# Performance work log

Measured on AMD Instinct MI355X. Metric: run time of the kernel, lower is better.

The kernel has to match this reference:

```python
import jax, jax.numpy as jnp
import numpy as np

DIM = 1024
HEADS = 16
DIM_HEAD = 64
INNER = HEADS * DIM_HEAD
N = 60  # 7 region tokens + 53 channel tokens
B = 512
NUM_FEATURES = 5
NUM_REGIONS = 7
REGIONS = [[1, 4, 10], [40, 47, 52], [2, 3, 5, 7, 8, 13], [44, 46, 49, 50, 51, 53],
           [6, 11, 14, 17, 18, 20, 25, 31, 32, 34, 39, 42, 45], [12, 24, 26, 38],
           [9, 15, 16, 19, 21, 22, 23, 27, 28, 29, 30, 33, 35, 36, 37, 41, 43, 48]]


def build_interaction_mask(n):
    m = np.zeros((n, n), dtype=bool)
    for r, chans in enumerate(REGIONS):
        ch = [c + 6 for c in chans]
        m[r, ch] = True
        m[ch, r] = True
    m[:NUM_REGIONS, :NUM_REGIONS] = True
    m[NUM_REGIONS:, NUM_REGIONS:] = True
    return jnp.asarray(m)


def setup_inputs() -> dict:
    key = jax.random.key(0)
    ks = jax.random.split(key, 9)
    s = 0.02
    return {
        "x": jax.random.normal(ks[0], (B, N, DIM), dtype=jnp.float32),
        # feature discretizer: 5 two-layer MLPs, stacked on leading axis
        "ext_w1": jax.random.normal(ks[1], (NUM_FEATURES, DIM, DIM // 2), dtype=jnp.float32) * s,
        "ext_b1": jnp.zeros((NUM_FEATURES, DIM // 2), dtype=jnp.float32),
        "ext_w2": jax.random.normal(ks[2], (NUM_FEATURES, DIM // 2), dtype=jnp.float32) * s,
        "ext_b2": jnp.zeros((NUM_FEATURES,), dtype=jnp.float32),
        # projections (stored input-major: y = x @ W)
        "qkv_w": jax.random.normal(ks[3], (DIM, 3 * INNER), dtype=jnp.float32) * s,
        "out_w": jax.random.normal(ks[4], (INNER, DIM), dtype=jnp.float32) * s,
        "out_b": jnp.zeros((DIM,), dtype=jnp.float32),
        "faw": jnp.ones((HEADS, NUM_FEATURES), dtype=jnp.float32),
    }


def reference(x, ext_w1, ext_b1, ext_w2, ext_b2, qkv_w, out_w, out_b, faw):
    b, n, d = x.shape
    scale = DIM_HEAD ** -0.5
    # feature discretizer: scores in (0,1), shape [b, n, 5]
    hmid = jax.nn.gelu(jnp.einsum('bnd,fdk->bfnk', x, ext_w1) + ext_b1[None, :, None, :],
                       approximate=False)
    feature_scores = jax.nn.sigmoid(
        jnp.einsum('bfnk,fk->bfn', hmid, ext_w2) + ext_b2[None, :, None]
    ).transpose(0, 2, 1)  # [b, n, f]
    # qkv
    qkv = x @ qkv_w  # [b, n, 3*inner]
    q, k, v = jnp.split(qkv, 3, axis=-1)
    to_heads = lambda t: t.reshape(b, n, HEADS, DIM_HEAD).transpose(0, 2, 1, 3)
    q, k, v = to_heads(q), to_heads(k), to_heads(v)
    dots = jnp.einsum('bhid,bhjd->bhij', q, k) * scale  # [b, h, n, n]
    # structured region-channel interaction mask (static)
    mask = build_interaction_mask(n)
    neg = -jnp.finfo(dots.dtype).max
    dots = jnp.where(mask[None, None, :, :], dots, neg)
    # per-head additive bias from discretized feature scores (row-wise, broadcast over j)
    fw = jax.nn.softmax(faw, axis=-1)  # [h, f]
    bias = jnp.einsum('bnf,hf->bhn', feature_scores, fw)[..., None]  # [b, h, n, 1]
    attn = jax.nn.softmax(dots + bias, axis=-1)
    out = jnp.einsum('bhij,bhjd->bhid', attn, v)
    out = out.transpose(0, 2, 1, 3).reshape(b, n, INNER)
    return out @ out_w + out_b
```

## Files before the change

### kernel.cpp

```cpp
#include <hip/hip_runtime.h>

typedef __bf16 bf16x8 __attribute__((ext_vector_type(8)));
typedef float f32x4 __attribute__((ext_vector_type(4)));

#define MFMA16(a, b, c) __builtin_amdgcn_mfma_f32_16x16x32_bf16(a, b, c, 0, 0, 0)

__device__ __forceinline__ void gload16(const __bf16* g, __bf16* l) {
    __builtin_amdgcn_global_load_lds(
        (const __attribute__((address_space(1))) void*)g,
        (__attribute__((address_space(3))) void*)l, 16, 0, 0);
}

__constant__ signed char CREG[54] = {
    -1,
    0, 2, 2, 0, 2, 4, 2, 2, 6, 0,
    4, 5, 2, 4, 6, 6, 4, 4, 6, 4,
    6, 6, 6, 5, 4, 5, 6, 6, 6, 6,
    4, 4, 6, 4, 6, 6, 6, 5, 4, 1,
    6, 4, 6, 3, 4, 3, 1, 6, 3, 3,
    3, 1, 3
};

__device__ __forceinline__ bool mask_ij(int i, int j) {
    if (i >= 60) return j == 0;
    if (j >= 60) return false;
    bool ri = i < 7, rj = j < 7;
    if (ri == rj) return true;
    if (ri) return CREG[j - 6] == i;
    return CREG[i - 6] == j;
}

__global__ __launch_bounds__(256) void prep(const float* __restrict__ x,
                                            __bf16* __restrict__ xb,
                                            const float* __restrict__ qkv_w,
                                            __bf16* __restrict__ qwt,
                                            const float* __restrict__ out_w,
                                            __bf16* __restrict__ owt) {
    __shared__ __bf16 t[64][65];
    const int bid = blockIdx.x;
    if (bid < 4096) {
        const int n8 = 31457280 / 8;
        int idx = bid * 256 + threadIdx.x;
        for (int i = idx; i < n8; i += 4096 * 256) {
            f32x4 a = *(const f32x4*)(x + (size_t)i * 8);
            f32x4 b = *(const f32x4*)(x + (size_t)i * 8 + 4);
            bf16x8 v;
            v[0] = (__bf16)a[0]; v[1] = (__bf16)a[1]; v[2] = (__bf16)a[2]; v[3] = (__bf16)a[3];
            v[4] = (__bf16)b[0]; v[5] = (__bf16)b[1]; v[6] = (__bf16)b[2]; v[7] = (__bf16)b[3];
            *(bf16x8*)(xb + (size_t)i * 8) = v;
        }
        return;
    }
    const float* in;
    __bf16* out;
    int R = 1024, C, tb;
    if (bid < 4864) { in = qkv_w; out = qwt; C = 3072; tb = bid - 4096; }
    else            { in = out_w; out = owt; C = 1024; tb = bid - 4864; }
    int ntc = C >> 6;
    int tr = tb / ntc, tc = tb % ntc;
    int r0 = tr * 64, c0 = tc * 64;
    for (int e = threadIdx.x; e < 4096; e += 256) {
        int r = e >> 6, c = e & 63;
        t[r][c] = (__bf16)in[(size_t)(r0 + r) * C + c0 + c];
    }
    __syncthreads();
    for (int e = threadIdx.x; e < 4096; e += 256) {
        int r = e >> 6, c = e & 63;
        out[(size_t)(c0 + r) * R + r0 + c] = t[c][r];
    }
}

#define BARRIER() __builtin_amdgcn_s_barrier()
#define LGKM0()                                                     \
    do {                                                            \
        asm volatile("s_waitcnt lgkmcnt(0)" ::: "memory");          \
        __builtin_amdgcn_sched_barrier(0);                          \
    } while (0)
#define VMC6() asm volatile("s_waitcnt vmcnt(6)" ::: "memory")
#define VMC0() asm volatile("s_waitcnt vmcnt(0)" ::: "memory")

#define ST_A(buf, mh, kt)                                                     \
    do {                                                                      \
        int r0_ = (mh) * 64 + wid * 8;                                        \
        int r1_ = 128 + (mh) * 64 + wid * 8;                                  \
        gload16(Ab + (size_t)(r0_ + srow) * K + (kt) + sslot * 8,             \
                &lds[buf][0][r0_][0]);                                        \
        gload16(Ab + (size_t)(r1_ + srow) * K + (kt) + sslot * 8,             \
                &lds[buf][0][r1_][0]);                                        \
    } while (0)

#define ST_B(buf, nh, kt)                                                     \
    do {                                                                      \
        int r0_ = (wid >> 2) * 64 + (nh) * 32 + (wid & 3) * 8;                \
        int r1_ = r0_ + 128;                                                  \
        gload16(Bb + (size_t)(r0_ + srow) * K + (kt) + sslot * 8,             \
                &lds[buf][1][r0_][0]);                                        \
        gload16(Bb + (size_t)(r1_ + srow) * K + (kt) + sslot * 8,             \
                &lds[buf][1][r1_][0]);                                        \
    } while (0)

#define RD_A(buf, mh)                                                         \
    _Pragma("unroll") for (int mq = 0; mq < 4; ++mq)                          \
    _Pragma("unroll") for (int kk = 0; kk < 2; ++kk)                          \
        af[(mh) * 4 + mq][kk] = *(const bf16x8*)(                             \
            &lds[buf][0][wm * 128 + ((mh) * 4 + mq) * 16 + lrow]              \
                [(((kk << 2) + hi) ^ (lrow & 7)) * 8]);

#define RD_B(buf, nh)                                                         \
    _Pragma("unroll") for (int nq = 0; nq < 2; ++nq)                          \
    _Pragma("unroll") for (int kk = 0; kk < 2; ++kk)                          \
        bfr[(nh) * 2 + nq][kk] = *(const bf16x8*)(                            \
            &lds[buf][1][wn * 64 + ((nh) * 2 + nq) * 16 + lrow]               \
                [(((kk << 2) + hi) ^ (lrow & 7)) * 8]);

#define QUAD(mh, nh)                                                          \
    do {                                                                      \
        __builtin_amdgcn_s_setprio(1);                                        \
        _Pragma("unroll") for (int mq = 0; mq < 4; ++mq)                      \
        _Pragma("unroll") for (int nq = 0; nq < 2; ++nq)                      \
        _Pragma("unroll") for (int kk = 0; kk < 2; ++kk)                      \
            acc[(mh) * 4 + mq][(nh) * 2 + nq] =                               \
                MFMA16(af[(mh) * 4 + mq][kk], bfr[(nh) * 2 + nq][kk],         \
                       acc[(mh) * 4 + mq][(nh) * 2 + nq]);                    \
        __builtin_amdgcn_s_setprio(0);                                        \
    } while (0)

template <int OUTF32>
__global__ __launch_bounds__(512, 2) void gemm256(const __bf16* __restrict__ A,
                                                  const __bf16* __restrict__ Bt,
                                                  __bf16* __restrict__ Cb,
                                                  float* __restrict__ Cf,
                                                  const float* __restrict__ bias,
                                                  int M, int N, int K) {
    __shared__ __align__(16) __bf16 lds[2][2][256][64];
    const int tid = threadIdx.x;
    const int wid = tid >> 6, lane = tid & 63;
    const int lrow = lane & 15, hi = lane >> 4;
    const int wm = wid >> 2, wn = wid & 3;

    const int ntn = N >> 8;
    const int nwg = gridDim.x, bid = blockIdx.x;
    const int swz = (bid & 7) * (nwg >> 3) + (bid >> 3);
    const int tm = swz / ntn, tn = swz % ntn;

    const __bf16* Ab = A + (size_t)tm * 256 * K;
    const __bf16* Bb = Bt + (size_t)tn * 256 * K;
    const int srow = lane >> 3;
    const int sslot = (lane & 7) ^ srow;

    f32x4 acc[8][4];
#pragma unroll
    for (int m = 0; m < 8; ++m)
#pragma unroll
        for (int n = 0; n < 4; ++n) acc[m][n] = 0;

    bf16x8 af[8][2], bfr[4][2];

    ST_A(0, 0, 0); ST_A(0, 1, 0); ST_B(0, 0, 0); ST_B(0, 1, 0);
    ST_A(1, 0, 64); ST_A(1, 1, 64); ST_B(1, 0, 64);
    VMC6();
    BARRIER();

    const int niter = K >> 7;
    for (int it = 0; it < niter; ++it) {
        const int kt1 = it * 128 + 64;
        const int ka = it * 128 + 128;
        const int kb = it * 128 + 192;
        const bool lastit = (it == niter - 1);

        RD_A(0, 0); RD_B(0, 0);
        ST_B(1, 1, kt1);
        BARRIER(); LGKM0(); QUAD(0, 0); BARRIER();
        RD_A(0, 1);
        if (!lastit) ST_A(0, 0, ka);
        BARRIER(); LGKM0(); QUAD(1, 0); BARRIER();
        RD_B(0, 1);
        if (!lastit) ST_A(0, 1, ka);
        BARRIER(); LGKM0(); QUAD(0, 1); BARRIER();
        if (!lastit) { ST_B(0, 0, ka); VMC6(); } else { VMC0(); }
        BARRIER(); LGKM0(); QUAD(1, 1); BARRIER();
        RD_A(1, 0); RD_B(1, 0);
        if (!lastit) ST_B(0, 1, ka);
        BARRIER(); LGKM0(); QUAD(0, 0); BARRIER();
        RD_A(1, 1);
        if (!lastit) ST_A(1, 0, kb);
        BARRIER(); LGKM0(); QUAD(1, 0); BARRIER();
        RD_B(1, 1);
        if (!lastit) ST_A(1, 1, kb);
        BARRIER(); LGKM0(); QUAD(0, 1); BARRIER();
        if (!lastit) { ST_B(1, 0, kb); VMC6(); }
        BARRIER(); LGKM0(); QUAD(1, 1); BARRIER();
    }

    VMC0();

#pragma unroll
    for (int m = 0; m < 8; ++m)
#pragma unroll
        for (int n = 0; n < 4; ++n) {
            int row = tm * 256 + wm * 128 + m * 16 + hi * 4;
            int col = tn * 256 + wn * 64 + n * 16 + lrow;
#pragma unroll
            for (int r = 0; r < 4; ++r) {
                if constexpr (OUTF32)
                    Cf[(size_t)(row + r) * N + col] = acc[m][n][r] + bias[col];
                else
                    Cb[(size_t)(row + r) * N + col] = (__bf16)acc[m][n][r];
            }
        }
}

__global__ __launch_bounds__(256) void attn_kernel(const __bf16* __restrict__ qkv,
                                                   __bf16* __restrict__ aout) {
    constexpr int LDK = 72;
    __shared__ __bf16 VT[64 * LDK];
    __shared__ __bf16 Ps[64 * LDK];

    const int b = blockIdx.x >> 4, h = blockIdx.x & 15;
    const int tid = threadIdx.x;
    const __bf16* base = qkv + (size_t)b * 60 * 3072 + h * 64;

    VT[(tid >> 2) * LDK + 60 + (tid & 3)] = (__bf16)0.f;

    for (int c = tid; c < 480; c += 256) {
        int n = c >> 3, d0 = (c & 7) * 8;
        bf16x8 v = *(const bf16x8*)(base + 2048 + (size_t)n * 3072 + d0);
#pragma unroll
        for (int j = 0; j < 8; ++j) VT[(d0 + j) * LDK + n] = v[j];
    }

    const int wid = tid >> 6, lane = tid & 63;
    const int lrow = lane & 15, hi = lane >> 4;
    const int wr = wid * 16;

    bf16x8 aq[2];
#pragma unroll
    for (int kk = 0; kk < 2; ++kk)
        aq[kk] = *(const bf16x8*)(base + (size_t)(wr + lrow) * 3072 + kk * 32 + hi * 8);

    f32x4 s[4];
#pragma unroll
    for (int fi = 0; fi < 4; ++fi) s[fi] = 0;
#pragma unroll
    for (int kk = 0; kk < 2; ++kk)
#pragma unroll
        for (int fi = 0; fi < 4; ++fi) {
            bf16x8 bk = *(const bf16x8*)(base + 1024 +
                                         (size_t)(fi * 16 + lrow) * 3072 +
                                         kk * 32 + hi * 8);
            s[fi] = MFMA16(aq[kk], bk, s[fi]);
        }

    const float scale = 0.125f;
#pragma unroll
    for (int r = 0; r < 4; ++r) {
        int i = wr + hi * 4 + r;
        float p[4];
        float mx = -3.0e38f;
#pragma unroll
        for (int fi = 0; fi < 4; ++fi) {
            int j = fi * 16 + lrow;
            float v = mask_ij(i, j) ? s[fi][r] * scale : -1.0e30f;
            p[fi] = v;
            mx = fmaxf(mx, v);
        }
#pragma unroll
        for (int off = 1; off <= 8; off <<= 1) mx = fmaxf(mx, __shfl_xor(mx, off));
        float se = 0.f;
#pragma unroll
        for (int fi = 0; fi < 4; ++fi) {
            p[fi] = __expf(p[fi] - mx);
            se += p[fi];
        }
#pragma unroll
        for (int off = 1; off <= 8; off <<= 1) se += __shfl_xor(se, off);
        float inv = 1.0f / se;
#pragma unroll
        for (int fi = 0; fi < 4; ++fi)
            Ps[i * LDK + fi * 16 + lrow] = (__bf16)(p[fi] * inv);
    }

    __syncthreads();

    f32x4 o[4];
#pragma unroll
    for (int fd = 0; fd < 4; ++fd) o[fd] = 0;
#pragma unroll
    for (int kk = 0; kk < 2; ++kk) {
        bf16x8 ap = *(const bf16x8*)(Ps + (wr + lrow) * LDK + kk * 32 + hi * 8);
#pragma unroll
        for (int fd = 0; fd < 4; ++fd) {
            bf16x8 bv = *(const bf16x8*)(VT + (fd * 16 + lrow) * LDK + kk * 32 + hi * 8);
            o[fd] = MFMA16(ap, bv, o[fd]);
        }
    }

#pragma unroll
    for (int fd = 0; fd < 4; ++fd)
#pragma unroll
        for (int r = 0; r < 4; ++r) {
            int i = wr + hi * 4 + r;
            if (i < 60)
                aout[(size_t)(b * 60 + i) * 1024 + h * 64 + fd * 16 + lrow] =
                    (__bf16)o[fd][r];
        }
}

extern "C" void kernel_launch(void* const* d_in, const int* in_sizes, int n_in,
                              void* d_out, int out_size, void* d_ws, size_t ws_size,
                              hipStream_t stream) {
    const float* x = (const float*)d_in[0];
    const float* qkv_w = (const float*)d_in[5];
    const float* out_w = (const float*)d_in[6];
    const float* out_b = (const float*)d_in[7];
    float* out = (float*)d_out;

    char* w = (char*)d_ws;
    __bf16* xb   = (__bf16*)w;
    __bf16* qwt  = (__bf16*)(w + 62914560);
    __bf16* owt  = (__bf16*)(w + 69206016);
    __bf16* qkv  = (__bf16*)(w + 71303168);
    __bf16* aout = (__bf16*)(w + 260046848);

    prep<<<dim3(5120), dim3(256), 0, stream>>>(x, xb, qkv_w, qwt, out_w, owt);

    gemm256<0><<<dim3(1440), dim3(512), 0, stream>>>(xb, qwt, qkv, nullptr,
                                                     nullptr, 30720, 3072, 1024);
    attn_kernel<<<dim3(512 * 16), dim3(256), 0, stream>>>(qkv, aout);

    gemm256<1><<<dim3(480), dim3(512), 0, stream>>>(aout, owt, nullptr, out,
                                                    out_b, 30720, 1024, 1024);
}
```

Before: 465.8 us.

## Shrink GEMM tile from 256x256 to 128x128 with 4-wave workgroups

Replaces the 256x256, 8-wave GEMM with a 128x128, 4-wave version, changing the LDS staging layout, fragment reads and launch grids (5760 and 1920 workgroups). The last-iteration branches are removed by clamping prefetch offsets to K-64, so redundant loads are issued instead of predicated ones. The aim is more workgroups for better CU load balance and occupancy. In exchange, operand reuse per tile drops, raising global and LDS traffic per FLOP.

```diff
diff --git a/kernel.cpp b/kernel.cpp
--- a/kernel.cpp
+++ b/kernel.cpp
@@ -81,8 +81,8 @@
 
 #define ST_A(buf, mh, kt)                                                     \
     do {                                                                      \
-        int r0_ = (mh) * 64 + wid * 8;                                        \
-        int r1_ = 128 + (mh) * 64 + wid * 8;                                  \
+        int r0_ = (mh) * 64 + wid * 16;                                       \
+        int r1_ = r0_ + 8;                                                    \
         gload16(Ab + (size_t)(r0_ + srow) * K + (kt) + sslot * 8,             \
                 &lds[buf][0][r0_][0]);                                        \
         gload16(Ab + (size_t)(r1_ + srow) * K + (kt) + sslot * 8,             \
@@ -91,8 +91,8 @@
 
 #define ST_B(buf, nh, kt)                                                     \
     do {                                                                      \
-        int r0_ = (wid >> 2) * 64 + (nh) * 32 + (wid & 3) * 8;                \
-        int r1_ = r0_ + 128;                                                  \
+        int r0_ = (nh) * 64 + wid * 16;                                       \
+        int r1_ = r0_ + 8;                                                    \
         gload16(Bb + (size_t)(r0_ + srow) * K + (kt) + sslot * 8,             \
                 &lds[buf][1][r0_][0]);                                        \
         gload16(Bb + (size_t)(r1_ + srow) * K + (kt) + sslot * 8,             \
@@ -100,10 +100,10 @@
     } while (0)
 
 #define RD_A(buf, mh)                                                         \
-    _Pragma("unroll") for (int mq = 0; mq < 4; ++mq)                          \
+    _Pragma("unroll") for (int mq = 0; mq < 2; ++mq)                          \
     _Pragma("unroll") for (int kk = 0; kk < 2; ++kk)                          \
-        af[(mh) * 4 + mq][kk] = *(const bf16x8*)(                             \
-            &lds[buf][0][wm * 128 + ((mh) * 4 + mq) * 16 + lrow]              \
+        af[(mh) * 2 + mq][kk] = *(const bf16x8*)(                             \
+            &lds[buf][0][wm * 64 + ((mh) * 2 + mq) * 16 + lrow]               \
                 [(((kk << 2) + hi) ^ (lrow & 7)) * 8]);
 
 #define RD_B(buf, nh)                                                         \
@@ -116,45 +116,45 @@
 #define QUAD(mh, nh)                                                          \
     do {                                                                      \
         __builtin_amdgcn_s_setprio(1);                                        \
-        _Pragma("unroll") for (int mq = 0; mq < 4; ++mq)                      \
+        _Pragma("unroll") for (int mq = 0; mq < 2; ++mq)                      \
         _Pragma("unroll") for (int nq = 0; nq < 2; ++nq)                      \
         _Pragma("unroll") for (int kk = 0; kk < 2; ++kk)                      \
-            acc[(mh) * 4 + mq][(nh) * 2 + nq] =                               \
-                MFMA16(af[(mh) * 4 + mq][kk], bfr[(nh) * 2 + nq][kk],         \
-                       acc[(mh) * 4 + mq][(nh) * 2 + nq]);                    \
+            acc[(mh) * 2 + mq][(nh) * 2 + nq] =                               \
+                MFMA16(af[(mh) * 2 + mq][kk], bfr[(nh) * 2 + nq][kk],         \
+                       acc[(mh) * 2 + mq][(nh) * 2 + nq]);                    \
         __builtin_amdgcn_s_setprio(0);                                        \
     } while (0)
 
 template <int OUTF32>
-__global__ __launch_bounds__(512, 2) void gemm256(const __bf16* __restrict__ A,
+__global__ __launch_bounds__(256, 2) void gemm128(const __bf16* __restrict__ A,
                                                   const __bf16* __restrict__ Bt,
                                                   __bf16* __restrict__ Cb,
                                                   float* __restrict__ Cf,
                                                   const float* __restrict__ bias,
                                                   int M, int N, int K) {
-    __shared__ __align__(16) __bf16 lds[2][2][256][64];
+    __shared__ __align__(16) __bf16 lds[2][2][128][64];
     const int tid = threadIdx.x;
     const int wid = tid >> 6, lane = tid & 63;
     const int lrow = lane & 15, hi = lane >> 4;
-    const int wm = wid >> 2, wn = wid & 3;
-
-    const int ntn = N >> 8;
+    const int wm = wid >> 1, wn = wid & 1;
+
+    const int ntn = N >> 7;
     const int nwg = gridDim.x, bid = blockIdx.x;
     const int swz = (bid & 7) * (nwg >> 3) + (bid >> 3);
     const int tm = swz / ntn, tn = swz % ntn;
 
-    const __bf16* Ab = A + (size_t)tm * 256 * K;
-    const __bf16* Bb = Bt + (size_t)tn * 256 * K;
+    const __bf16* Ab = A + (size_t)tm * 128 * K;
+    const __bf16* Bb = Bt + (size_t)tn * 128 * K;
     const int srow = lane >> 3;
     const int sslot = (lane & 7) ^ srow;
 
-    f32x4 acc[8][4];
-#pragma unroll
-    for (int m = 0; m < 8; ++m)
+    f32x4 acc[4][4];
+#pragma unroll
+    for (int m = 0; m < 4; ++m)
 #pragma unroll
         for (int n = 0; n < 4; ++n) acc[m][n] = 0;
 
-    bf16x8 af[8][2], bfr[4][2];
+    bf16x8 af[4][2], bfr[4][2];
 
     ST_A(0, 0, 0); ST_A(0, 1, 0); ST_B(0, 0, 0); ST_B(0, 1, 0);
     ST_A(1, 0, 64); ST_A(1, 1, 64); ST_B(1, 0, 64);
@@ -164,42 +164,44 @@
     const int niter = K >> 7;
     for (int it = 0; it < niter; ++it) {
         const int kt1 = it * 128 + 64;
-        const int ka = it * 128 + 128;
-        const int kb = it * 128 + 192;
-        const bool lastit = (it == niter - 1);
+        const int ka = (it * 128 + 128 < K) ? it * 128 + 128 : K - 64;
+        const int kb = (kt1 + 128 < K) ? kt1 + 128 : K - 64;
 
         RD_A(0, 0); RD_B(0, 0);
         ST_B(1, 1, kt1);
         BARRIER(); LGKM0(); QUAD(0, 0); BARRIER();
         RD_A(0, 1);
-        if (!lastit) ST_A(0, 0, ka);
+        ST_A(0, 0, ka);
         BARRIER(); LGKM0(); QUAD(1, 0); BARRIER();
         RD_B(0, 1);
-        if (!lastit) ST_A(0, 1, ka);
+        ST_A(0, 1, ka);
         BARRIER(); LGKM0(); QUAD(0, 1); BARRIER();
-        if (!lastit) { ST_B(0, 0, ka); VMC6(); } else { VMC0(); }
+        ST_B(0, 0, ka);
+        VMC6();
         BARRIER(); LGKM0(); QUAD(1, 1); BARRIER();
         RD_A(1, 0); RD_B(1, 0);
-        if (!lastit) ST_B(0, 1, ka);
+        ST_B(0, 1, ka);
         BARRIER(); LGKM0(); QUAD(0, 0); BARRIER();
         RD_A(1, 1);
-        if (!lastit) ST_A(1, 0, kb);
+        ST_A(1, 0, kb);
         BARRIER(); LGKM0(); QUAD(1, 0); BARRIER();
         RD_B(1, 1);
-        if (!lastit) ST_A(1, 1, kb);
+        ST_A(1, 1, kb);
         BARRIER(); LGKM0(); QUAD(0, 1); BARRIER();
-        if (!lastit) { ST_B(1, 0, kb); VMC6(); }
+        ST_B(1, 0, kb);
+        VMC6();
         BARRIER(); LGKM0(); QUAD(1, 1); BARRIER();
     }
 
     VMC0();
-
-#pragma unroll
-    for (int m = 0; m < 8; ++m)
+    BARRIER();
+
+#pragma unroll
+    for (int m = 0; m < 4; ++m)
 #pragma unroll
         for (int n = 0; n < 4; ++n) {
-            int row = tm * 256 + wm * 128 + m * 16 + hi * 4;
-            int col = tn * 256 + wn * 64 + n * 16 + lrow;
+            int row = tm * 128 + wm * 64 + m * 16 + hi * 4;
+            int col = tn * 128 + wn * 64 + n * 16 + lrow;
 #pragma unroll
             for (int r = 0; r < 4; ++r) {
                 if constexpr (OUTF32)
@@ -324,10 +326,10 @@
 
     prep<<<dim3(5120), dim3(256), 0, stream>>>(x, xb, qkv_w, qwt, out_w, owt);
 
-    gemm256<0><<<dim3(1440), dim3(512), 0, stream>>>(xb, qwt, qkv, nullptr,
+    gemm128<0><<<dim3(5760), dim3(256), 0, stream>>>(xb, qwt, qkv, nullptr,
                                                      nullptr, 30720, 3072, 1024);
     attn_kernel<<<dim3(512 * 16), dim3(256), 0, stream>>>(qkv, aout);
 
-    gemm256<1><<<dim3(480), dim3(512), 0, stream>>>(aout, owt, nullptr, out,
-                                                    out_b, 30720, 1024, 1024);
-}
+    gemm128<1><<<dim3(1920), dim3(256), 0, stream>>>(aout, owt, nullptr, out,
+                                                     out_b, 30720, 1024, 1024);
+}
```

After: 425.1 us. -8.7%, faster.
